# Optimization experiments

Hardware: AMD Instinct MI355X
Metric: run time of the kernel (lower is better)

Reference implementation:

```python
import jax, jax.numpy as jnp
import numpy as np

D_MODEL = 1024
NHEAD = 16
HEAD_DIM = D_MODEL // NHEAD
HID = int(D_MODEL * 4.0 * (2.0 / 3.0))  # 2730, matches int(d_model*mlp_ratio*2/3)
EPS = 1e-5


def setup_inputs() -> dict:
    key = jax.random.key(0)
    ks = jax.random.split(key, 12)
    s = lambda fi, fo: (2.0 / (fi + fo)) ** 0.5
    inp = {
        "x": jax.random.normal(ks[0], (2, 2048, D_MODEL), dtype=jnp.float32),
        "ln1_w": jnp.ones((D_MODEL,), jnp.float32),
        "ln1_b": jnp.zeros((D_MODEL,), jnp.float32),
        "wq": jax.random.normal(ks[1], (D_MODEL, D_MODEL), jnp.float32) * s(D_MODEL, D_MODEL),
        "wk": jax.random.normal(ks[2], (D_MODEL, D_MODEL), jnp.float32) * s(D_MODEL, D_MODEL),
        "wv": jax.random.normal(ks[3], (D_MODEL, D_MODEL), jnp.float32) * s(D_MODEL, D_MODEL),
        "wg": jax.random.normal(ks[4], (D_MODEL, D_MODEL), jnp.float32) * s(D_MODEL, D_MODEL),
        "wo": jax.random.normal(ks[5], (D_MODEL, D_MODEL), jnp.float32) * s(D_MODEL, D_MODEL),
        "ln2_w": jnp.ones((D_MODEL,), jnp.float32),
        "ln2_b": jnp.zeros((D_MODEL,), jnp.float32),
        "w_in": jax.random.normal(ks[6], (D_MODEL, 2 * HID), jnp.float32) * s(D_MODEL, 2 * HID),
        "b_in": jnp.zeros((2 * HID,), jnp.float32),
        "w_out": jax.random.normal(ks[7], (HID, D_MODEL), jnp.float32) * s(HID, D_MODEL),
        "b_out": jnp.zeros((D_MODEL,), jnp.float32),
    }
    return inp


def _layernorm(x, w, b):
    mu = jnp.mean(x, axis=-1, keepdims=True)
    var = jnp.var(x, axis=-1, keepdims=True)
    return (x - mu) * jax.lax.rsqrt(var + EPS) * w + b


def _decay_matrix(S):
    # gamma_h = 1 - 2^{-5-h}, RetNet multiscale decays
    gamma = 1.0 - jnp.exp2(-5.0 - jnp.arange(NHEAD, dtype=jnp.float32))  # [H]
    n = jnp.arange(S, dtype=jnp.float32)
    exp = n[:, None] - n[None, :]                     # [S, S]
    mask = exp >= 0
    d = gamma[:, None, None] ** jnp.where(mask, exp, 0.0)  # [H, S, S]
    return jnp.where(mask[None], d, 0.0)


def _msr(xn, wq, wk, wv, wg, wo):
    B, S, _ = xn.shape
    split = lambda t: t.reshape(B, S, NHEAD, HEAD_DIM).transpose(0, 2, 1, 3)  # bhsd
    q = split(xn @ wq) * (HEAD_DIM ** -0.5)
    k = split(xn @ wk)
    v = split(xn @ wv)
    Dm = _decay_matrix(S)                                   # [H, S, S]
    scores = jnp.einsum("bhsd,bhtd->bhst", q, k) * Dm[None]  # causal decayed retention
    out = jnp.einsum("bhst,bhtd->bhsd", scores, v)
    # per-head normalization (GroupNorm over head dim, no affine)
    mu = jnp.mean(out, axis=-1, keepdims=True)
    var = jnp.var(out, axis=-1, keepdims=True)
    out = (out - mu) * jax.lax.rsqrt(var + 1e-6)
    out = out.transpose(0, 2, 1, 3).reshape(B, S, D_MODEL)
    out = out * jax.nn.silu(xn @ wg)                        # swish gate
    return out @ wo


def _swiglu(x, w_in, b_in, w_out, b_out):
    ab = x @ w_in + b_in
    a, b = ab[..., :HID], ab[..., HID:]
    return (a * jax.nn.silu(b)) @ w_out + b_out


def reference(x, ln1_w, ln1_b, wq, wk, wv, wg, wo, ln2_w, ln2_b, w_in, b_in, w_out, b_out):
    h = _msr(_layernorm(x, ln1_w, ln1_b), wq, wk, wv, wg, wo)
    x = x + h  # dropout/drop_path identity at eval
    x = x + _swiglu(_layernorm(x, ln2_w, ln2_b), w_in, b_in, w_out, b_out)
    return x
```

## Files before the change

kernel.cpp:

```cpp
#include <hip/hip_runtime.h>
#include <math.h>

#define D_MODEL 1024
#define NHEAD   16
#define HDIM    64
#define HID     2730
#define HID_PAD 2816
#define SEQ     2048
#define BATCH   2
#define NTOK    (BATCH * SEQ)
#define QKG     3072

typedef __attribute__((ext_vector_type(8))) short bf16x8;
typedef __attribute__((ext_vector_type(4))) float f32x4;
typedef __attribute__((ext_vector_type(4))) short s16x4;

static __device__ inline short f2bf(float f)
{
    union { float f; unsigned int u; } c; c.f = f;
    unsigned int r = c.u + 0x7FFFu + ((c.u >> 16) & 1u);
    return (short)(r >> 16);
}
static __device__ inline float bf2f(short s)
{
    union { unsigned int u; float f; } c;
    c.u = ((unsigned int)(unsigned short)s) << 16;
    return c.f;
}

#define GLD16(gsrc, ldst) \
    __builtin_amdgcn_global_load_lds((const __attribute__((address_space(1))) void*)(gsrc), \
                                     (__attribute__((address_space(3))) void*)(ldst), 16, 0, 0)

__global__ void ln_kernel(const float* __restrict__ x,
                          const float* __restrict__ w,
                          const float* __restrict__ b,
                          short* __restrict__ out,
                          float eps)
{
    int row = blockIdx.x;
    int t = threadIdx.x;
    const float4* xr = (const float4*)(x + (size_t)row * D_MODEL);
    float4 v = xr[t];
    float s  = v.x + v.y + v.z + v.w;
    float sq = v.x * v.x + v.y * v.y + v.z * v.z + v.w * v.w;
#pragma unroll
    for (int off = 32; off > 0; off >>= 1) {
        s  += __shfl_xor(s, off);
        sq += __shfl_xor(sq, off);
    }
    __shared__ float ss[4], ssq[4];
    int wave = t >> 6;
    if ((t & 63) == 0) { ss[wave] = s; ssq[wave] = sq; }
    __syncthreads();
    s  = ss[0] + ss[1] + ss[2] + ss[3];
    sq = ssq[0] + ssq[1] + ssq[2] + ssq[3];
    float mu  = s * (1.0f / D_MODEL);
    float var = sq * (1.0f / D_MODEL) - mu * mu;
    float inv = rsqrtf(var + eps);
    float4 wv = ((const float4*)w)[t];
    float4 bv = ((const float4*)b)[t];
    s16x4 o;
    o.x = f2bf((v.x - mu) * inv * wv.x + bv.x);
    o.y = f2bf((v.y - mu) * inv * wv.y + bv.y);
    o.z = f2bf((v.z - mu) * inv * wv.z + bv.z);
    o.w = f2bf((v.w - mu) * inv * wv.w + bv.w);
    *(s16x4*)(out + (size_t)row * D_MODEL + 4 * t) = o;
}

__global__ void transpose_f2b(const float* __restrict__ src, int ldsrc, int coloff,
                              int nvalid, int kvalid, int KPAD,
                              short* __restrict__ dst)
{
    __shared__ float tile[32][33];
    int k0 = blockIdx.x * 32, n0 = blockIdx.y * 32;
    int tx = threadIdx.x, ty = threadIdx.y;
#pragma unroll
    for (int i = 0; i < 32; i += 8) {
        int k = k0 + ty + i, n = n0 + tx;
        tile[ty + i][tx] = (k < kvalid && n < nvalid) ? src[(size_t)k * ldsrc + coloff + n] : 0.0f;
    }
    __syncthreads();
#pragma unroll
    for (int i = 0; i < 32; i += 8) {
        int n = n0 + ty + i, k = k0 + tx;
        dst[(size_t)n * KPAD + k] = f2bf(tile[tx][ty + i]);
    }
}

template<int EPI>
__global__ __launch_bounds__(256) void gemm_bt(
        const short* __restrict__ A, int lda,
        const short* __restrict__ Bt,
        const float* __restrict__ bias,
        const float* __restrict__ R, int ldr,
        void* __restrict__ C, int ldc, int K)
{
    __shared__ short As[2][4096];
    __shared__ short Bs[2][4096];
    int bm = blockIdx.y * 128;
    int bn = blockIdx.x * 128;
    int t = threadIdx.x;
    int w = t >> 6;
    int lane = t & 63;
    int quad = lane >> 4;
    int l15  = lane & 15;

    const short* gA0 = A  + (size_t)(bm + (t >> 2)) * lda + ((t & 3) << 3);
    const short* gA1 = gA0 + (size_t)64 * lda;
    const short* gB0 = Bt + (size_t)(bn + (t >> 2)) * K + ((t & 3) << 3);
    const short* gB1 = gB0 + (size_t)64 * K;
    int wb = w << 9;

    int wr = (w >> 1) * 64;
    int wc = (w & 1) * 64;

    f32x4 acc[4][4];
#pragma unroll
    for (int i = 0; i < 4; ++i)
#pragma unroll
        for (int j = 0; j < 4; ++j) acc[i][j] = (f32x4){0.f, 0.f, 0.f, 0.f};

    GLD16(gA0, &As[0][wb]);
    GLD16(gA1, &As[0][2048 + wb]);
    GLD16(gB0, &Bs[0][wb]);
    GLD16(gB1, &Bs[0][2048 + wb]);

    for (int k0 = 0; k0 < K; k0 += 32) {
        int cur = (k0 >> 5) & 1;
        __syncthreads();
        int k1 = k0 + 32;
        if (k1 < K) {
            GLD16(gA0 + k1, &As[cur ^ 1][wb]);
            GLD16(gA1 + k1, &As[cur ^ 1][2048 + wb]);
            GLD16(gB0 + k1, &Bs[cur ^ 1][wb]);
            GLD16(gB1 + k1, &Bs[cur ^ 1][2048 + wb]);
        }
        bf16x8 af[4], bfr[4];
#pragma unroll
        for (int i = 0; i < 4; ++i)
            af[i] = *(const bf16x8*)(&As[cur][(wr + i * 16 + l15) * 32 + quad * 8]);
#pragma unroll
        for (int j = 0; j < 4; ++j)
            bfr[j] = *(const bf16x8*)(&Bs[cur][(wc + j * 16 + l15) * 32 + quad * 8]);
#pragma unroll
        for (int i = 0; i < 4; ++i)
#pragma unroll
            for (int j = 0; j < 4; ++j)
                acc[i][j] = __builtin_amdgcn_mfma_f32_16x16x32_bf16(af[i], bfr[j], acc[i][j], 0, 0, 0);
    }

#pragma unroll
    for (int i = 0; i < 4; ++i) {
        int gr = bm + wr + i * 16 + quad * 4;
#pragma unroll
        for (int j = 0; j < 4; ++j) {
            int gc = bn + wc + j * 16 + l15;
#pragma unroll
            for (int r = 0; r < 4; ++r) {
                float val = acc[i][j][r];
                size_t idx = (size_t)(gr + r) * ldc + gc;
                if (EPI == 0) {
                    ((short*)C)[idx] = f2bf(val);
                } else if (EPI == 1) {
                    ((float*)C)[idx] = val + R[(size_t)(gr + r) * ldr + gc];
                } else {
                    ((float*)C)[idx] = val + bias[gc] + R[(size_t)(gr + r) * ldr + gc];
                }
            }
        }
    }
}

__global__ __launch_bounds__(256) void mlp_fused(
        const short* __restrict__ A,
        const short* __restrict__ w_inT,
        const float* __restrict__ b_in,
        short* __restrict__ hm)
{
    __shared__ short As[2][4096];
    __shared__ short Ba[2][2048];
    __shared__ short Bb[2][2048];
    const int K = D_MODEL;
    int bm = blockIdx.y * 128;
    int bn = blockIdx.x * 64;
    int t = threadIdx.x;
    int w = t >> 6;
    int lane = t & 63;
    int quad = lane >> 4;
    int l15  = lane & 15;

    const short* gA0 = A + (size_t)(bm + (t >> 2)) * K + ((t & 3) << 3);
    const short* gA1 = gA0 + (size_t)64 * K;
    const short* gBa = w_inT + (size_t)(bn + (t >> 2)) * K + ((t & 3) << 3);
    const short* gBb = gBa + (size_t)HID_PAD * K;
    int wb = w << 9;

    int wr = (w >> 1) * 64;
    int wc = (w & 1) * 32;

    f32x4 acca[4][2], accb[4][2];
#pragma unroll
    for (int i = 0; i < 4; ++i)
#pragma unroll
        for (int j = 0; j < 2; ++j) {
            acca[i][j] = (f32x4){0.f, 0.f, 0.f, 0.f};
            accb[i][j] = (f32x4){0.f, 0.f, 0.f, 0.f};
        }

    GLD16(gA0, &As[0][wb]);
    GLD16(gA1, &As[0][2048 + wb]);
    GLD16(gBa, &Ba[0][wb]);
    GLD16(gBb, &Bb[0][wb]);

    for (int k0 = 0; k0 < K; k0 += 32) {
        int cur = (k0 >> 5) & 1;
        __syncthreads();
        int k1 = k0 + 32;
        if (k1 < K) {
            GLD16(gA0 + k1, &As[cur ^ 1][wb]);
            GLD16(gA1 + k1, &As[cur ^ 1][2048 + wb]);
            GLD16(gBa + k1, &Ba[cur ^ 1][wb]);
            GLD16(gBb + k1, &Bb[cur ^ 1][wb]);
        }
        bf16x8 af[4], baf[2], bbf[2];
#pragma unroll
        for (int i = 0; i < 4; ++i)
            af[i] = *(const bf16x8*)(&As[cur][(wr + i * 16 + l15) * 32 + quad * 8]);
#pragma unroll
        for (int j = 0; j < 2; ++j) {
            baf[j] = *(const bf16x8*)(&Ba[cur][(wc + j * 16 + l15) * 32 + quad * 8]);
            bbf[j] = *(const bf16x8*)(&Bb[cur][(wc + j * 16 + l15) * 32 + quad * 8]);
        }
#pragma unroll
        for (int i = 0; i < 4; ++i)
#pragma unroll
            for (int j = 0; j < 2; ++j) {
                acca[i][j] = __builtin_amdgcn_mfma_f32_16x16x32_bf16(af[i], baf[j], acca[i][j], 0, 0, 0);
                accb[i][j] = __builtin_amdgcn_mfma_f32_16x16x32_bf16(af[i], bbf[j], accb[i][j], 0, 0, 0);
            }
    }

#pragma unroll
    for (int i = 0; i < 4; ++i) {
        int gr = bm + wr + i * 16 + quad * 4;
#pragma unroll
        for (int j = 0; j < 2; ++j) {
            int gc = bn + wc + j * 16 + l15;
            bool ok = gc < HID;
            float ba = ok ? b_in[gc] : 0.0f;
            float bb = ok ? b_in[HID + gc] : 0.0f;
#pragma unroll
            for (int r = 0; r < 4; ++r) {
                float a  = acca[i][j][r] + ba;
                float bv = accb[i][j][r] + bb;
                float val = ok ? a * (bv / (1.0f + expf(-bv))) : 0.0f;
                hm[(size_t)(gr + r) * HID_PAD + gc] = f2bf(val);
            }
        }
    }
}

#define PSTR 72

__global__ __launch_bounds__(512) void retention_mfma(
        const short* __restrict__ qkg,
        const short* __restrict__ vT,
        short* __restrict__ rg)
{
    int qb = (int)gridDim.x - 1 - (int)blockIdx.x;
    int h  = blockIdx.y;
    int b  = blockIdx.z;

    __shared__ short ks[2][4096];
    __shared__ short vt[2][4096];
    __shared__ short ps[8][16 * PSTR];

    int tid  = threadIdx.x;
    int w    = tid >> 6;
    int lane = tid & 63;
    int quad = lane >> 4;
    int l15  = lane & 15;

    float log2g = log1pf(-exp2f(-5.0f - (float)h)) * 1.4426950408889634f;
    int hcol = h * HDIM;
    int s0 = qb * 128;
    size_t tok0 = (size_t)b * SEQ;

    int sch  = tid >> 8;
    int srow = (tid >> 2) & 63;
    int sp8  = (tid & 3) << 3;
    const short* kbase  = qkg + (tok0 + srow) * QKG + 1024 + hcol + sch * 32 + sp8;
    const short* vtbase = vT + (size_t)(hcol + srow) * NTOK + tok0 + sch * 32 + sp8;
    int lb = tid << 3;

    const short* qrow = qkg + (tok0 + s0 + w * 16 + l15) * QKG + hcol;
    bf16x8 qa0 = *(const bf16x8*)(qrow + quad * 8);
    bf16x8 qa1 = *(const bf16x8*)(qrow + 32 + quad * 8);

    float colfac[4];
#pragma unroll
    for (int tile = 0; tile < 4; ++tile)
        colfac[tile] = exp2f(-(float)(tile * 16 + l15) * log2g) * 0.125f;

    f32x4 oacc[4];
#pragma unroll
    for (int i = 0; i < 4; ++i) oacc[i] = (f32x4){0.f, 0.f, 0.f, 0.f};

    int sbase = s0 + w * 16 + quad * 4;
    int tmax = 2 * qb + 1;

    GLD16(kbase, &ks[0][lb]);
    GLD16(vtbase, &vt[0][lb]);

    for (int tb = 0; tb <= tmax; ++tb) {
        int cur = tb & 1;
        __syncthreads();
        if (tb < tmax) {
            GLD16(kbase + (size_t)(tb + 1) * 64 * QKG, &ks[cur ^ 1][lb]);
            GLD16(vtbase + (tb + 1) * 64, &vt[cur ^ 1][lb]);
        }

        f32x4 sacc[4];
#pragma unroll
        for (int i = 0; i < 4; ++i) sacc[i] = (f32x4){0.f, 0.f, 0.f, 0.f};
#pragma unroll
        for (int tile = 0; tile < 4; ++tile) {
            bf16x8 kb0 = *(const bf16x8*)(&ks[cur][(tile * 16 + l15) * 32 + quad * 8]);
            bf16x8 kb1 = *(const bf16x8*)(&ks[cur][2048 + (tile * 16 + l15) * 32 + quad * 8]);
            sacc[tile] = __builtin_amdgcn_mfma_f32_16x16x32_bf16(qa0, kb0, sacc[tile], 0, 0, 0);
            sacc[tile] = __builtin_amdgcn_mfma_f32_16x16x32_bf16(qa1, kb1, sacc[tile], 0, 0, 0);
        }

        int fbi = sbase - tb * 64;
        float rf[4];
#pragma unroll
        for (int reg = 0; reg < 4; ++reg)
            rf[reg] = exp2f((float)(fbi + reg) * log2g);

        if (tb * 64 + 63 > s0 + w * 16) {
#pragma unroll
            for (int tile = 0; tile < 4; ++tile) {
                int tt = tile * 16 + l15;
#pragma unroll
                for (int reg = 0; reg < 4; ++reg) {
                    float p = (fbi + reg >= tt) ? sacc[tile][reg] * rf[reg] * colfac[tile] : 0.0f;
                    ps[w][(quad * 4 + reg) * PSTR + tile * 16 + l15] = f2bf(p);
                }
            }
        } else {
#pragma unroll
            for (int tile = 0; tile < 4; ++tile)
#pragma unroll
                for (int reg = 0; reg < 4; ++reg)
                    ps[w][(quad * 4 + reg) * PSTR + tile * 16 + l15] =
                        f2bf(sacc[tile][reg] * (rf[reg] * colfac[tile]));
        }

#pragma unroll
        for (int ksi = 0; ksi < 2; ++ksi) {
            bf16x8 pa = *(const bf16x8*)(&ps[w][l15 * PSTR + ksi * 32 + quad * 8]);
#pragma unroll
            for (int dt = 0; dt < 4; ++dt) {
                bf16x8 vb = *(const bf16x8*)(&vt[cur][ksi * 2048 + (dt * 16 + l15) * 32 + quad * 8]);
                oacc[dt] = __builtin_amdgcn_mfma_f32_16x16x32_bf16(pa, vb, oacc[dt], 0, 0, 0);
            }
        }
    }

    float s1[4], s2[4];
#pragma unroll
    for (int reg = 0; reg < 4; ++reg) {
        s1[reg] = oacc[0][reg] + oacc[1][reg] + oacc[2][reg] + oacc[3][reg];
        s2[reg] = oacc[0][reg] * oacc[0][reg] + oacc[1][reg] * oacc[1][reg]
                + oacc[2][reg] * oacc[2][reg] + oacc[3][reg] * oacc[3][reg];
    }
#pragma unroll
    for (int off = 1; off < 16; off <<= 1) {
#pragma unroll
        for (int reg = 0; reg < 4; ++reg) {
            s1[reg] += __shfl_xor(s1[reg], off);
            s2[reg] += __shfl_xor(s2[reg], off);
        }
    }
    size_t rowtok = tok0 + s0 + w * 16 + quad * 4;
    short* obase = rg + rowtok * D_MODEL + hcol;
    const short* gbase = qkg + rowtok * QKG + 2048 + hcol;
#pragma unroll
    for (int reg = 0; reg < 4; ++reg) {
        float mu  = s1[reg] * (1.0f / 64.0f);
        float var = s2[reg] * (1.0f / 64.0f) - mu * mu;
        float inv = rsqrtf(var + 1e-6f);
#pragma unroll
        for (int dt = 0; dt < 4; ++dt) {
            float gv = bf2f(gbase[(size_t)reg * QKG + dt * 16 + l15]);
            float val = (oacc[dt][reg] - mu) * inv * (gv / (1.0f + expf(-gv)));
            obase[(size_t)reg * D_MODEL + dt * 16 + l15] = f2bf(val);
        }
    }
}

extern "C" void kernel_launch(void* const* d_in, const int* in_sizes, int n_in,
                              void* d_out, int out_size, void* d_ws, size_t ws_size,
                              hipStream_t stream)
{
    const float* x     = (const float*)d_in[0];
    const float* ln1w  = (const float*)d_in[1];
    const float* ln1b  = (const float*)d_in[2];
    const float* wq    = (const float*)d_in[3];
    const float* wk    = (const float*)d_in[4];
    const float* wv    = (const float*)d_in[5];
    const float* wg    = (const float*)d_in[6];
    const float* wo    = (const float*)d_in[7];
    const float* ln2w  = (const float*)d_in[8];
    const float* ln2b  = (const float*)d_in[9];
    const float* w_in  = (const float*)d_in[10];
    const float* b_in  = (const float*)d_in[11];
    const float* w_out = (const float*)d_in[12];
    const float* b_out = (const float*)d_in[13];
    float* out = (float*)d_out;
    char* base = (char*)d_ws;

    const size_t MB = 1u << 20;
    short* xn     = (short*)(base);
    short* qkgT   = (short*)(base +  8 * MB);
    short* wvT    = (short*)(base + 14 * MB);
    short* woT    = (short*)(base + 16 * MB);
    short* w_inT  = (short*)(base + 18 * MB);
    short* w_outT = (short*)(base + 29 * MB);
    short* qkg    = (short*)(base + 35 * MB);
    short* hm     = (short*)(base + 35 * MB);
    short* vT     = (short*)(base + 59 * MB);
    short* rg     = (short*)(base + 67 * MB);

    dim3 tb(32, 8);
    transpose_f2b<<<dim3(32, 32), tb, 0, stream>>>(wq, 1024, 0, 1024, 1024, 1024, qkgT);
    transpose_f2b<<<dim3(32, 32), tb, 0, stream>>>(wk, 1024, 0, 1024, 1024, 1024, qkgT + 1024 * 1024);
    transpose_f2b<<<dim3(32, 32), tb, 0, stream>>>(wg, 1024, 0, 1024, 1024, 1024, qkgT + 2 * 1024 * 1024);
    transpose_f2b<<<dim3(32, 32), tb, 0, stream>>>(wv, 1024, 0, 1024, 1024, 1024, wvT);
    transpose_f2b<<<dim3(32, 32), tb, 0, stream>>>(wo, 1024, 0, 1024, 1024, 1024, woT);
    transpose_f2b<<<dim3(32, 88), tb, 0, stream>>>(w_in, 2 * HID, 0,   HID, 1024, 1024, w_inT);
    transpose_f2b<<<dim3(32, 88), tb, 0, stream>>>(w_in, 2 * HID, HID, HID, 1024, 1024, w_inT + (size_t)HID_PAD * 1024);
    transpose_f2b<<<dim3(88, 32), tb, 0, stream>>>(w_out, 1024, 0, 1024, HID, HID_PAD, w_outT);

    ln_kernel<<<NTOK, 256, 0, stream>>>(x, ln1w, ln1b, xn, 1e-5f);
    gemm_bt<0><<<dim3(QKG / 128, 32), 256, 0, stream>>>(xn, D_MODEL, qkgT, nullptr, nullptr, 0, qkg, QKG, D_MODEL);
    gemm_bt<0><<<dim3(NTOK / 128, 8), 256, 0, stream>>>(wvT, D_MODEL, xn, nullptr, nullptr, 0, vT, NTOK, D_MODEL);
    retention_mfma<<<dim3(SEQ / 128, NHEAD, BATCH), 512, 0, stream>>>(qkg, vT, rg);
    gemm_bt<1><<<dim3(8, 32), 256, 0, stream>>>(rg, D_MODEL, woT, nullptr, x, D_MODEL, out, D_MODEL, D_MODEL);
    ln_kernel<<<NTOK, 256, 0, stream>>>(out, ln2w, ln2b, xn, 1e-5f);
    mlp_fused<<<dim3(HID_PAD / 64, NTOK / 128), 256, 0, stream>>>(xn, w_inT, b_in, hm);
    gemm_bt<2><<<dim3(8, 32), 256, 0, stream>>>(hm, HID_PAD, w_outT, b_out, out, D_MODEL, out, D_MODEL, HID_PAD);
}
```

Baseline: 442.9 us.

## Batch weight transposes, merge projection GEMMs, and swap grid order for reuse

Replaces eight separate weight transpose launches with one batched transpose kernel that uses 64x64 tiles and vectorized bf16 stores. Merges the QKG and V projection GEMMs into one launch of 1024 blocks. Reorders the grid for the output-projection, MLP and down-projection kernels so consecutive blocks walk along M and share the same weight tile in cache. The aim is to cut launch overhead and improve L2 reuse of weights. The batched transpose launches many blocks that exit early, and its strided LDS reads may cause bank conflicts.

```diff
diff --git a/kernel.cpp b/kernel.cpp
--- a/kernel.cpp
+++ b/kernel.cpp
@@ -68,38 +68,56 @@
     *(s16x4*)(out + (size_t)row * D_MODEL + 4 * t) = o;
 }
 
-__global__ void transpose_f2b(const float* __restrict__ src, int ldsrc, int coloff,
-                              int nvalid, int kvalid, int KPAD,
-                              short* __restrict__ dst)
-{
-    __shared__ float tile[32][33];
-    int k0 = blockIdx.x * 32, n0 = blockIdx.y * 32;
-    int tx = threadIdx.x, ty = threadIdx.y;
-#pragma unroll
-    for (int i = 0; i < 32; i += 8) {
-        int k = k0 + ty + i, n = n0 + tx;
-        tile[ty + i][tx] = (k < kvalid && n < nvalid) ? src[(size_t)k * ldsrc + coloff + n] : 0.0f;
+struct TJob {
+    const float* src;
+    short* dst;
+    int ldsrc, coloff, nvalid, kvalid, KPAD, NPAD;
+};
+struct TJobs { TJob j[8]; };
+
+__global__ __launch_bounds__(256) void transpose_all(TJobs jobs)
+{
+    TJob jb = jobs.j[blockIdx.z];
+    int k0 = blockIdx.x * 64, n0 = blockIdx.y * 64;
+    if (k0 >= jb.KPAD || n0 >= jb.NPAD) return;
+    __shared__ float tile[64][65];
+    int t = threadIdx.x;
+    {
+        int kk = t >> 2, np = (t & 3) << 4;
+        int k = k0 + kk;
+        bool kok = k < jb.kvalid;
+        const float* srow = jb.src + (size_t)k * jb.ldsrc + jb.coloff + n0 + np;
+#pragma unroll
+        for (int i = 0; i < 16; ++i) {
+            int n = n0 + np + i;
+            tile[kk][np + i] = (kok && n < jb.nvalid) ? srow[i] : 0.0f;
+        }
     }
     __syncthreads();
-#pragma unroll
-    for (int i = 0; i < 32; i += 8) {
-        int n = n0 + ty + i, k = k0 + tx;
-        dst[(size_t)n * KPAD + k] = f2bf(tile[tx][ty + i]);
+    {
+        int nn = t >> 2, kp = (t & 3) << 4;
+        short* drow = jb.dst + (size_t)(n0 + nn) * jb.KPAD + k0 + kp;
+#pragma unroll
+        for (int v4 = 0; v4 < 4; ++v4) {
+            s16x4 o;
+            o.x = f2bf(tile[kp + v4 * 4 + 0][nn]);
+            o.y = f2bf(tile[kp + v4 * 4 + 1][nn]);
+            o.z = f2bf(tile[kp + v4 * 4 + 2][nn]);
+            o.w = f2bf(tile[kp + v4 * 4 + 3][nn]);
+            *(s16x4*)(drow + v4 * 4) = o;
+        }
     }
 }
 
 template<int EPI>
-__global__ __launch_bounds__(256) void gemm_bt(
+static __device__ __forceinline__ void gemm_core(
         const short* __restrict__ A, int lda,
         const short* __restrict__ Bt,
         const float* __restrict__ bias,
         const float* __restrict__ R, int ldr,
-        void* __restrict__ C, int ldc, int K)
-{
-    __shared__ short As[2][4096];
-    __shared__ short Bs[2][4096];
-    int bm = blockIdx.y * 128;
-    int bn = blockIdx.x * 128;
+        void* __restrict__ C, int ldc, int K, int bm, int bn,
+        short (*As)[4096], short (*Bs)[4096])
+{
     int t = threadIdx.x;
     int w = t >> 6;
     int lane = t & 63;
@@ -172,6 +190,40 @@
     }
 }
 
+template<int EPI>
+__global__ __launch_bounds__(256) void gemm_swz(
+        const short* __restrict__ A, int lda,
+        const short* __restrict__ Bt,
+        const float* __restrict__ bias,
+        const float* __restrict__ R, int ldr,
+        void* __restrict__ C, int ldc, int K)
+{
+    __shared__ short As[2][4096];
+    __shared__ short Bs[2][4096];
+    gemm_core<EPI>(A, lda, Bt, bias, R, ldr, C, ldc, K,
+                   blockIdx.x * 128, blockIdx.y * 128, As, Bs);
+}
+
+__global__ __launch_bounds__(256) void proj_kernel(
+        const short* __restrict__ xn,
+        const short* __restrict__ qkgT,
+        short* __restrict__ qkg,
+        const short* __restrict__ wvT,
+        short* __restrict__ vT)
+{
+    __shared__ short As[2][4096];
+    __shared__ short Bs[2][4096];
+    int id = blockIdx.x;
+    if (id < 768) {
+        int bm = (id & 31) * 128, bn = (id >> 5) * 128;
+        gemm_core<0>(xn, D_MODEL, qkgT, nullptr, nullptr, 0, qkg, QKG, D_MODEL, bm, bn, As, Bs);
+    } else {
+        int i2 = id - 768;
+        int bn = (i2 & 31) * 128, bm = (i2 >> 5) * 128;
+        gemm_core<0>(wvT, D_MODEL, xn, nullptr, nullptr, 0, vT, NTOK, D_MODEL, bm, bn, As, Bs);
+    }
+}
+
 __global__ __launch_bounds__(256) void mlp_fused(
         const short* __restrict__ A,
         const short* __restrict__ w_inT,
@@ -182,8 +234,8 @@
     __shared__ short Ba[2][2048];
     __shared__ short Bb[2][2048];
     const int K = D_MODEL;
-    int bm = blockIdx.y * 128;
-    int bn = blockIdx.x * 64;
+    int bm = blockIdx.x * 128;
+    int bn = blockIdx.y * 64;
     int t = threadIdx.x;
     int w = t >> 6;
     int lane = t & 63;
@@ -433,22 +485,22 @@
     short* vT     = (short*)(base + 59 * MB);
     short* rg     = (short*)(base + 67 * MB);
 
-    dim3 tb(32, 8);
-    transpose_f2b<<<dim3(32, 32), tb, 0, stream>>>(wq, 1024, 0, 1024, 1024, 1024, qkgT);
-    transpose_f2b<<<dim3(32, 32), tb, 0, stream>>>(wk, 1024, 0, 1024, 1024, 1024, qkgT + 1024 * 1024);
-    transpose_f2b<<<dim3(32, 32), tb, 0, stream>>>(wg, 1024, 0, 1024, 1024, 1024, qkgT + 2 * 1024 * 1024);
-    transpose_f2b<<<dim3(32, 32), tb, 0, stream>>>(wv, 1024, 0, 1024, 1024, 1024, wvT);
-    transpose_f2b<<<dim3(32, 32), tb, 0, stream>>>(wo, 1024, 0, 1024, 1024, 1024, woT);
-    transpose_f2b<<<dim3(32, 88), tb, 0, stream>>>(w_in, 2 * HID, 0,   HID, 1024, 1024, w_inT);
-    transpose_f2b<<<dim3(32, 88), tb, 0, stream>>>(w_in, 2 * HID, HID, HID, 1024, 1024, w_inT + (size_t)HID_PAD * 1024);
-    transpose_f2b<<<dim3(88, 32), tb, 0, stream>>>(w_out, 1024, 0, 1024, HID, HID_PAD, w_outT);
+    TJobs jobs;
+    jobs.j[0] = { wq,    qkgT,                          1024,    0, 1024, 1024, 1024, 1024 };
+    jobs.j[1] = { wk,    qkgT + 1024 * 1024,            1024,    0, 1024, 1024, 1024, 1024 };
+    jobs.j[2] = { wg,    qkgT + 2 * 1024 * 1024,        1024,    0, 1024, 1024, 1024, 1024 };
+    jobs.j[3] = { wv,    wvT,                           1024,    0, 1024, 1024, 1024, 1024 };
+    jobs.j[4] = { wo,    woT,                           1024,    0, 1024, 1024, 1024, 1024 };
+    jobs.j[5] = { w_in,  w_inT,                         2 * HID, 0,   HID, 1024, 1024, HID_PAD };
+    jobs.j[6] = { w_in,  w_inT + (size_t)HID_PAD * 1024, 2 * HID, HID, HID, 1024, 1024, HID_PAD };
+    jobs.j[7] = { w_out, w_outT,                        1024,    0, 1024, HID, HID_PAD, 1024 };
+    transpose_all<<<dim3(44, 44, 8), 256, 0, stream>>>(jobs);
 
     ln_kernel<<<NTOK, 256, 0, stream>>>(x, ln1w, ln1b, xn, 1e-5f);
-    gemm_bt<0><<<dim3(QKG / 128, 32), 256, 0, stream>>>(xn, D_MODEL, qkgT, nullptr, nullptr, 0, qkg, QKG, D_MODEL);
-    gemm_bt<0><<<dim3(NTOK / 128, 8), 256, 0, stream>>>(wvT, D_MODEL, xn, nullptr, nullptr, 0, vT, NTOK, D_MODEL);
+    proj_kernel<<<1024, 256, 0, stream>>>(xn, qkgT, qkg, wvT, vT);
     retention_mfma<<<dim3(SEQ / 128, NHEAD, BATCH), 512, 0, stream>>>(qkg, vT, rg);
-    gemm_bt<1><<<dim3(8, 32), 256, 0, stream>>>(rg, D_MODEL, woT, nullptr, x, D_MODEL, out, D_MODEL, D_MODEL);
+    gemm_swz<1><<<dim3(32, 8), 256, 0, stream>>>(rg, D_MODEL, woT, nullptr, x, D_MODEL, out, D_MODEL, D_MODEL);
     ln_kernel<<<NTOK, 256, 0, stream>>>(out, ln2w, ln2b, xn, 1e-5f);
-    mlp_fused<<<dim3(HID_PAD / 64, NTOK / 128), 256, 0, stream>>>(xn, w_inT, b_in, hm);
-    gemm_bt<2><<<dim3(8, 32), 256, 0, stream>>>(hm, HID_PAD, w_outT, b_out, out, D_MODEL, out, D_MODEL, HID_PAD);
-}
+    mlp_fused<<<dim3(NTOK / 128, HID_PAD / 64), 256, 0, stream>>>(xn, w_inT, b_in, hm);
+    gemm_swz<2><<<dim3(32, 8), 256, 0, stream>>>(hm, HID_PAD, w_outT, b_out, out, D_MODEL, out, D_MODEL, HID_PAD);
+}
```

Result: faster. 433.5 us (-2.1%).
